# Kernel tuning notes

Hardware: AMD Instinct MI355X
Metric: run time of the kernel (lower is better)

The kernel has to match this reference:

```python
import jax, jax.numpy as jnp
import numpy as np

MARGIN = 0.5  # forward body overrides self.margin = 0.5 inside the loop


def setup_inputs() -> dict:
    key = jax.random.key(0)
    k1, k2 = jax.random.split(key)
    B, H, W = 8, 64, 64
    pred_weights = jax.random.normal(k1, (B, H, W), dtype=jnp.float32)
    true_mask = jax.random.uniform(k2, (B, H, W), dtype=jnp.float32)
    return {"pred_weights": pred_weights, "true_mask": true_mask}


def reference(pred_weights, true_mask):
    B = pred_weights.shape[0]
    x = pred_weights.reshape(B, -1)          # [B, N], N = H*W
    m = true_mask.reshape(B, -1)
    # per-sample max normalization (torch.max over flattened sample)
    x = x / jnp.max(x, axis=1, keepdims=True)
    pos_m = (m > 0.5).astype(x.dtype)        # [B, N]
    neg_m = (m < 0.5).astype(x.dtype)
    # masked pairwise margin: relu(margin - (pos_i - neg_j)) over pos x neg pairs
    diff = MARGIN - (x[:, :, None] - x[:, None, :])  # [B, N, N]
    w = pos_m[:, :, None] * neg_m[:, None, :]        # pair validity mask
    per_sample = jnp.sum(jax.nn.relu(diff) * w, axis=(1, 2))  # [B]
    n_pos = jnp.sum(pos_m, axis=1)
    n_neg = jnp.sum(neg_m, axis=1)
    denom = n_pos * n_neg + 1e-8
    valid = (n_pos > 0) & (n_neg > 0)        # skip samples with empty pos/neg
    sample_loss = jnp.where(valid, per_sample / denom, 0.0)
    # reduction == 'mean' divides by batch size
    return jnp.sum(sample_loss) / B
```

## Files before the change

kernel.cpp:

```cpp
#include <hip/hip_runtime.h>

#define BATCH 8
#define N 4096
#define TPB 512
#define SPB 32
#define NBLK (BATCH * SPB)
#define COMB_SZ 4104

__global__ __launch_bounds__(TPB) void srs_fused_kernel(
    const float* __restrict__ pred,
    const float* __restrict__ mask,
    float* __restrict__ out,
    float* __restrict__ partials,
    unsigned int* __restrict__ cnt)
{
    int b   = blockIdx.x >> 5;
    int c   = blockIdx.x & 31;
    int tid = threadIdx.x;
    int lane = tid & 63;
    int wid  = tid >> 6;
    const float* xb = pred + b * N;
    const float* mb = mask + b * N;

    __shared__ float4 comb4[COMB_SZ / 4];
    float* comb = (float*)comb4;
    __shared__ float red[8];
    __shared__ int   ctr[2];
    __shared__ float srmax;
    __shared__ int   sLast;

    const float4* xb4 = (const float4*)xb;
    const float4* mb4 = (const float4*)mb;
    float lmax = -3.4e38f;
#pragma unroll
    for (int e = 0; e < N / 4 / TPB; ++e) {
        float4 v = xb4[tid + e * TPB];
        lmax = fmaxf(fmaxf(lmax, fmaxf(v.x, v.y)), fmaxf(v.z, v.w));
    }
    for (int off = 32; off > 0; off >>= 1)
        lmax = fmaxf(lmax, __shfl_down(lmax, off));
    if (lane == 0) red[wid] = lmax;
    if (tid == 0) { ctr[0] = 0; ctr[1] = 0; }
    __syncthreads();
    if (tid == 0) {
        float mx = red[0];
#pragma unroll
        for (int w = 1; w < 8; ++w) mx = fmaxf(mx, red[w]);
        srmax = 1.0f / mx;
    }
    __syncthreads();
    float rmax = srmax;

#pragma unroll
    for (int e = 0; e < N / 4 / TPB; ++e) {
        float4 xv = xb4[tid + e * TPB];
        float4 mv = mb4[tid + e * TPB];
        float xs[4] = {xv.x, xv.y, xv.z, xv.w};
        float ms[4] = {mv.x, mv.y, mv.z, mv.w};
#pragma unroll
        for (int q = 0; q < 4; ++q) {
            float nv = xs[q] * rmax;
            bool isp = ms[q] > 0.5f;
            bool isn = ms[q] < 0.5f;
            unsigned long long bp = __ballot(isp);
            unsigned long long bn = __ballot(isn);
            int basep = 0, basen = 0;
            if (lane == 0) {
                basep = atomicAdd(&ctr[0], __popcll(bp));
                basen = atomicAdd(&ctr[1], __popcll(bn));
            }
            basep = __shfl(basep, 0);
            basen = __shfl(basen, 0);
            unsigned long long lower = (1ull << lane) - 1ull;
            if (isp) comb[COMB_SZ - 1 - (basep + __popcll(bp & lower))] = nv;
            if (isn) comb[basen + __popcll(bn & lower)] = nv + 0.5f;
        }
    }
    __syncthreads();
    int npos = ctr[0], nneg = ctr[1];
    int nneg4 = (nneg + 3) & ~3;
    if (tid < nneg4 - nneg) comb[nneg + tid] = -1.0e30f;
    __syncthreads();

    int ii = tid & 63;
    int jsplit = tid >> 6;
    int nj4 = nneg4 >> 2;
    float a0 = 0.f, a1 = 0.f, a2 = 0.f, a3 = 0.f;
    for (int ip = c * 64 + ii; ip < npos; ip += SPB * 64) {
        float xi = comb[COMB_SZ - 1 - ip];
#pragma unroll 4
        for (int j4 = jsplit; j4 < nj4; j4 += 8) {
            float4 v = comb4[j4];
            a0 += fmaxf(v.x - xi, 0.f);
            a1 += fmaxf(v.y - xi, 0.f);
            a2 += fmaxf(v.z - xi, 0.f);
            a3 += fmaxf(v.w - xi, 0.f);
        }
    }
    float acc = (a0 + a1) + (a2 + a3);
    for (int off = 32; off > 0; off >>= 1) acc += __shfl_down(acc, off);
    __syncthreads();
    if (lane == 0) red[wid] = acc;
    __syncthreads();

    if (tid == 0) {
        float tot = 0.f;
#pragma unroll
        for (int w = 0; w < 8; ++w) tot += red[w];
        float denom = (float)npos * (float)nneg + 1e-8f;
        float scale = (npos > 0 && nneg > 0) ? 1.0f / (denom * (float)BATCH) : 0.0f;
        __hip_atomic_store(&partials[blockIdx.x], tot * scale,
                           __ATOMIC_RELEASE, __HIP_MEMORY_SCOPE_AGENT);
        unsigned int old = __hip_atomic_fetch_add(cnt, 1u, __ATOMIC_ACQ_REL,
                                                  __HIP_MEMORY_SCOPE_AGENT);
        sLast = (((old + 1u) & (NBLK - 1u)) == 0u) ? 1 : 0;
    }
    __syncthreads();
    if (sLast && wid == 0) {
        float s = 0.f;
#pragma unroll
        for (int k = 0; k < NBLK / 64; ++k)
            s += __hip_atomic_load(&partials[lane + 64 * k],
                                   __ATOMIC_ACQUIRE, __HIP_MEMORY_SCOPE_AGENT);
        for (int off = 32; off > 0; off >>= 1) s += __shfl_down(s, off);
        if (lane == 0)
            __hip_atomic_store(out, s, __ATOMIC_RELEASE, __HIP_MEMORY_SCOPE_AGENT);
    }
}

extern "C" void kernel_launch(void* const* d_in, const int* in_sizes, int n_in,
                              void* d_out, int out_size, void* d_ws, size_t ws_size,
                              hipStream_t stream) {
    const float* pred = (const float*)d_in[0];
    const float* mask = (const float*)d_in[1];
    float* out = (float*)d_out;
    float* partials = (float*)d_ws;
    unsigned int* cnt = (unsigned int*)((char*)d_ws + NBLK * sizeof(float));

    srs_fused_kernel<<<NBLK, TPB, 0, stream>>>(pred, mask, out, partials, cnt);
}
```

Before: 18.70 us.

## Iterate over the smaller of the pos/neg sets, with register-held inputs and batched ballots

Pos and neg values are now stored in separate sentinel-padded halves of shared memory. The pairwise loop puts two fixed elements per thread on the smaller set and streams over the larger one, which removes the per-block strided loop over npos and the padding pass. Each thread loads its inputs once and keeps them in registers. The per-element ballot atomics are reduced to a single shared atomic per wave. The extra syncthreads and the shared max broadcast are gone, the finalisation runs per wave, and the final partial loads are relaxed. The code relies on sentinels (±1e30) to null out unused slots, and each block covers exactly 64 of the smaller set's elements, which assumes that set holds at most 2048 items.

```diff
diff --git a/kernel.cpp b/kernel.cpp
--- a/kernel.cpp
+++ b/kernel.cpp
@@ -5,7 +5,9 @@
 #define TPB 512
 #define SPB 32
 #define NBLK (BATCH * SPB)
-#define COMB_SZ 4104
+#define POS_F 4096
+#define SENT_NEG -1.0e30f
+#define SENT_POS  1.0e30f
 
 __global__ __launch_bounds__(TPB) void srs_fused_kernel(
     const float* __restrict__ pred,
@@ -14,117 +16,137 @@
     float* __restrict__ partials,
     unsigned int* __restrict__ cnt)
 {
-    int b   = blockIdx.x >> 5;
-    int c   = blockIdx.x & 31;
-    int tid = threadIdx.x;
-    int lane = tid & 63;
-    int wid  = tid >> 6;
-    const float* xb = pred + b * N;
-    const float* mb = mask + b * N;
+    const int b    = blockIdx.x >> 5;
+    const int c    = blockIdx.x & 31;
+    const int tid  = threadIdx.x;
+    const int lane = tid & 63;
+    const int wid  = tid >> 6;
 
-    __shared__ float4 comb4[COMB_SZ / 4];
+    __shared__ float4 comb4[2048];
     float* comb = (float*)comb4;
     __shared__ float red[8];
-    __shared__ int   ctr[2];
-    __shared__ float srmax;
-    __shared__ int   sLast;
+    __shared__ int ctr[2];
 
-    const float4* xb4 = (const float4*)xb;
-    const float4* mb4 = (const float4*)mb;
-    float lmax = -3.4e38f;
-#pragma unroll
-    for (int e = 0; e < N / 4 / TPB; ++e) {
-        float4 v = xb4[tid + e * TPB];
-        lmax = fmaxf(fmaxf(lmax, fmaxf(v.x, v.y)), fmaxf(v.z, v.w));
-    }
+    const float4* xb4 = (const float4*)(pred + b * N);
+    const float4* mb4 = (const float4*)(mask + b * N);
+
+    float4 xv0 = xb4[tid];
+    float4 xv1 = xb4[tid + 512];
+    float4 mv0 = mb4[tid];
+    float4 mv1 = mb4[tid + 512];
+
+    comb4[tid]        = make_float4(SENT_NEG, SENT_NEG, SENT_NEG, SENT_NEG);
+    comb4[tid + 512]  = make_float4(SENT_NEG, SENT_NEG, SENT_NEG, SENT_NEG);
+    comb4[tid + 1024] = make_float4(SENT_POS, SENT_POS, SENT_POS, SENT_POS);
+    comb4[tid + 1536] = make_float4(SENT_POS, SENT_POS, SENT_POS, SENT_POS);
+    if (tid < 2) ctr[tid] = 0;
+
+    float lmax = fmaxf(fmaxf(xv0.x, xv0.y), fmaxf(xv0.z, xv0.w));
+    lmax = fmaxf(lmax, fmaxf(fmaxf(xv1.x, xv1.y), fmaxf(xv1.z, xv1.w)));
     for (int off = 32; off > 0; off >>= 1)
         lmax = fmaxf(lmax, __shfl_down(lmax, off));
     if (lane == 0) red[wid] = lmax;
-    if (tid == 0) { ctr[0] = 0; ctr[1] = 0; }
     __syncthreads();
-    if (tid == 0) {
-        float mx = red[0];
+
+    float mx = red[0];
 #pragma unroll
-        for (int w = 1; w < 8; ++w) mx = fmaxf(mx, red[w]);
-        srmax = 1.0f / mx;
+    for (int w = 1; w < 8; ++w) mx = fmaxf(mx, red[w]);
+    const float rmax = 1.0f / mx;
+
+    float xs[8] = {xv0.x, xv0.y, xv0.z, xv0.w, xv1.x, xv1.y, xv1.z, xv1.w};
+    float ms[8] = {mv0.x, mv0.y, mv0.z, mv0.w, mv1.x, mv1.y, mv1.z, mv1.w};
+    bool isp[8], isn[8];
+    unsigned long long bp[8], bn[8];
+#pragma unroll
+    for (int k = 0; k < 8; ++k) {
+        isp[k] = ms[k] > 0.5f;
+        isn[k] = ms[k] < 0.5f;
+        bp[k] = __ballot(isp[k]);
+        bn[k] = __ballot(isn[k]);
+    }
+    int cp = 0, cn = 0;
+#pragma unroll
+    for (int k = 0; k < 8; ++k) { cp += (int)__popcll(bp[k]); cn += (int)__popcll(bn[k]); }
+    int basep = 0, basen = 0;
+    if (lane == 0) {
+        basep = atomicAdd(&ctr[0], cp);
+        basen = atomicAdd(&ctr[1], cn);
+    }
+    basep = __shfl(basep, 0);
+    basen = __shfl(basen, 0);
+    const unsigned long long lower = (1ull << lane) - 1ull;
+    int op = 0, on = 0;
+#pragma unroll
+    for (int k = 0; k < 8; ++k) {
+        float nv = xs[k] * rmax;
+        if (isp[k]) comb[POS_F + basep + op + (int)__popcll(bp[k] & lower)] = nv;
+        if (isn[k]) comb[basen + on + (int)__popcll(bn[k] & lower)] = nv + 0.5f;
+        op += (int)__popcll(bp[k]);
+        on += (int)__popcll(bn[k]);
     }
     __syncthreads();
-    float rmax = srmax;
 
-#pragma unroll
-    for (int e = 0; e < N / 4 / TPB; ++e) {
-        float4 xv = xb4[tid + e * TPB];
-        float4 mv = mb4[tid + e * TPB];
-        float xs[4] = {xv.x, xv.y, xv.z, xv.w};
-        float ms[4] = {mv.x, mv.y, mv.z, mv.w};
-#pragma unroll
-        for (int q = 0; q < 4; ++q) {
-            float nv = xs[q] * rmax;
-            bool isp = ms[q] > 0.5f;
-            bool isn = ms[q] < 0.5f;
-            unsigned long long bp = __ballot(isp);
-            unsigned long long bn = __ballot(isn);
-            int basep = 0, basen = 0;
-            if (lane == 0) {
-                basep = atomicAdd(&ctr[0], __popcll(bp));
-                basen = atomicAdd(&ctr[1], __popcll(bn));
-            }
-            basep = __shfl(basep, 0);
-            basen = __shfl(basen, 0);
-            unsigned long long lower = (1ull << lane) - 1ull;
-            if (isp) comb[COMB_SZ - 1 - (basep + __popcll(bp & lower))] = nv;
-            if (isn) comb[basen + __popcll(bn & lower)] = nv + 0.5f;
+    const int npos = ctr[0], nneg = ctr[1];
+    const int ii = tid & 31;
+    const int jsplit = tid >> 5;
+    float a0=0.f,a1=0.f,a2=0.f,a3=0.f,a4=0.f,a5=0.f,a6=0.f,a7=0.f;
+
+    if (npos <= nneg) {
+        const float xiA = comb[POS_F + c * 64 + ii];
+        const float xiB = comb[POS_F + c * 64 + ii + 32];
+        const int nj4 = (nneg + 3) >> 2;
+#pragma unroll 2
+        for (int j4 = jsplit; j4 < nj4; j4 += 16) {
+            float4 v = comb4[j4];
+            a0 += fmaxf(v.x - xiA, 0.f); a1 += fmaxf(v.y - xiA, 0.f);
+            a2 += fmaxf(v.z - xiA, 0.f); a3 += fmaxf(v.w - xiA, 0.f);
+            a4 += fmaxf(v.x - xiB, 0.f); a5 += fmaxf(v.y - xiB, 0.f);
+            a6 += fmaxf(v.z - xiB, 0.f); a7 += fmaxf(v.w - xiB, 0.f);
+        }
+    } else {
+        const float wjA = comb[c * 64 + ii];
+        const float wjB = comb[c * 64 + ii + 32];
+        const int nj4 = (npos + 3) >> 2;
+#pragma unroll 2
+        for (int j4 = jsplit; j4 < nj4; j4 += 16) {
+            float4 v = comb4[1024 + j4];
+            a0 += fmaxf(wjA - v.x, 0.f); a1 += fmaxf(wjA - v.y, 0.f);
+            a2 += fmaxf(wjA - v.z, 0.f); a3 += fmaxf(wjA - v.w, 0.f);
+            a4 += fmaxf(wjB - v.x, 0.f); a5 += fmaxf(wjB - v.y, 0.f);
+            a6 += fmaxf(wjB - v.z, 0.f); a7 += fmaxf(wjB - v.w, 0.f);
         }
     }
-    __syncthreads();
-    int npos = ctr[0], nneg = ctr[1];
-    int nneg4 = (nneg + 3) & ~3;
-    if (tid < nneg4 - nneg) comb[nneg + tid] = -1.0e30f;
-    __syncthreads();
-
-    int ii = tid & 63;
-    int jsplit = tid >> 6;
-    int nj4 = nneg4 >> 2;
-    float a0 = 0.f, a1 = 0.f, a2 = 0.f, a3 = 0.f;
-    for (int ip = c * 64 + ii; ip < npos; ip += SPB * 64) {
-        float xi = comb[COMB_SZ - 1 - ip];
-#pragma unroll 4
-        for (int j4 = jsplit; j4 < nj4; j4 += 8) {
-            float4 v = comb4[j4];
-            a0 += fmaxf(v.x - xi, 0.f);
-            a1 += fmaxf(v.y - xi, 0.f);
-            a2 += fmaxf(v.z - xi, 0.f);
-            a3 += fmaxf(v.w - xi, 0.f);
-        }
-    }
-    float acc = (a0 + a1) + (a2 + a3);
+    float acc = ((a0 + a1) + (a2 + a3)) + ((a4 + a5) + (a6 + a7));
     for (int off = 32; off > 0; off >>= 1) acc += __shfl_down(acc, off);
-    __syncthreads();
     if (lane == 0) red[wid] = acc;
     __syncthreads();
 
-    if (tid == 0) {
+    if (wid == 0) {
         float tot = 0.f;
 #pragma unroll
         for (int w = 0; w < 8; ++w) tot += red[w];
-        float denom = (float)npos * (float)nneg + 1e-8f;
-        float scale = (npos > 0 && nneg > 0) ? 1.0f / (denom * (float)BATCH) : 0.0f;
-        __hip_atomic_store(&partials[blockIdx.x], tot * scale,
-                           __ATOMIC_RELEASE, __HIP_MEMORY_SCOPE_AGENT);
-        unsigned int old = __hip_atomic_fetch_add(cnt, 1u, __ATOMIC_ACQ_REL,
-                                                  __HIP_MEMORY_SCOPE_AGENT);
-        sLast = (((old + 1u) & (NBLK - 1u)) == 0u) ? 1 : 0;
-    }
-    __syncthreads();
-    if (sLast && wid == 0) {
-        float s = 0.f;
+        const float denom = (float)npos * (float)nneg + 1e-8f;
+        const float scale = (npos > 0 && nneg > 0) ? 1.0f / (denom * (float)BATCH) : 0.0f;
+        const float part = tot * scale;
+        int last = 0;
+        if (lane == 0) {
+            __hip_atomic_store(&partials[blockIdx.x], part,
+                               __ATOMIC_RELEASE, __HIP_MEMORY_SCOPE_AGENT);
+            unsigned int old = __hip_atomic_fetch_add(cnt, 1u, __ATOMIC_ACQ_REL,
+                                                      __HIP_MEMORY_SCOPE_AGENT);
+            last = (((old + 1u) & (NBLK - 1u)) == 0u) ? 1 : 0;
+        }
+        last = __shfl(last, 0);
+        if (last) {
+            float s = 0.f;
 #pragma unroll
-        for (int k = 0; k < NBLK / 64; ++k)
-            s += __hip_atomic_load(&partials[lane + 64 * k],
-                                   __ATOMIC_ACQUIRE, __HIP_MEMORY_SCOPE_AGENT);
-        for (int off = 32; off > 0; off >>= 1) s += __shfl_down(s, off);
-        if (lane == 0)
-            __hip_atomic_store(out, s, __ATOMIC_RELEASE, __HIP_MEMORY_SCOPE_AGENT);
+            for (int k = 0; k < NBLK / 64; ++k)
+                s += __hip_atomic_load(&partials[lane + 64 * k],
+                                       __ATOMIC_RELAXED, __HIP_MEMORY_SCOPE_AGENT);
+            for (int off = 32; off > 0; off >>= 1) s += __shfl_down(s, off);
+            if (lane == 0)
+                __hip_atomic_store(out, s, __ATOMIC_RELEASE, __HIP_MEMORY_SCOPE_AGENT);
+        }
     }
 }
 
```

Result: faster. 17.48 us (-6.5%).
